# Kernel tuning notes

Hardware: AMD Instinct MI355X
Metric: run time of the kernel (lower is better)

Reference implementation:

```python
import jax, jax.numpy as jnp
import numpy as np

B, TD, ND, FD, H = 16384, 256, 256, 512, 8
HID = [512, 256]


def _ln(x, g, b, eps=1e-5):
    m = jnp.mean(x, -1, keepdims=True)
    v = jnp.mean((x - m) ** 2, -1, keepdims=True)
    return (x - m) * jax.lax.rsqrt(v + eps) * g + b


def _mha1(q_in, k_in, v_in, wq, bq, wk, bk, wv, bv, wo, bo):
    # MultiheadAttention with seq_len=1 on both sides; eval mode (dropout off).
    Bq, E = q_in.shape
    dh = E // H
    q = (q_in @ wq.T + bq).reshape(Bq, H, dh)
    k = (k_in @ wk.T + bk).reshape(Bq, H, dh)
    scores = jnp.sum(q * k, -1) / np.sqrt(dh)          # [B, H]
    w = jax.nn.softmax(scores[..., None], axis=-1)      # [B, H, 1] -> exactly 1 (single key)
    attn = jnp.mean(w, axis=1)[:, None, :]              # averaged over heads -> [B, 1, 1]
    v = v_in @ wv.T + bv                                # attn weight == 1, so attn_out == v
    out = v @ wo.T + bo
    return out, attn


def setup_inputs():
    key = jax.random.key(0)
    ks = iter(jax.random.split(key, 40))
    def p(*shape):
        return jax.random.normal(next(ks), shape, dtype=jnp.float32) * 0.02
    inp = {
        'text_emb': jax.random.normal(next(ks), (B, TD), dtype=jnp.float32),
        'num_emb': jax.random.normal(next(ks), (B, ND), dtype=jnp.float32),
        'tp_w': p(FD, TD), 'tp_b': p(FD),
        'np_w': p(FD, ND), 'np_b': p(FD),
        'a1_wq': p(FD, FD), 'a1_wk': p(FD, FD), 'a1_wv': p(FD, FD),
        'a1_bq': p(FD), 'a1_bk': p(FD), 'a1_bv': p(FD),
        'a1_wo': p(FD, FD), 'a1_bo': p(FD),
        'a2_wq': p(FD, FD), 'a2_wk': p(FD, FD), 'a2_wv': p(FD, FD),
        'a2_bq': p(FD), 'a2_bk': p(FD), 'a2_bv': p(FD),
        'a2_wo': p(FD, FD), 'a2_bo': p(FD),
        'n1_g': jnp.ones((FD,), jnp.float32), 'n1_b': jnp.zeros((FD,), jnp.float32),
        'n2_g': jnp.ones((FD,), jnp.float32), 'n2_b': jnp.zeros((FD,), jnp.float32),
        'g_w': p(FD, 2 * FD), 'g_b': p(FD),
        'm1_w': p(HID[0], 2 * FD), 'm1_b': p(HID[0]),
        'ln1_g': jnp.ones((HID[0],), jnp.float32), 'ln1_b': jnp.zeros((HID[0],), jnp.float32),
        'm2_w': p(HID[1], HID[0]), 'm2_b': p(HID[1]),
        'ln2_g': jnp.ones((HID[1],), jnp.float32), 'ln2_b': jnp.zeros((HID[1],), jnp.float32),
    }
    return inp


def reference(text_emb, num_emb, tp_w, tp_b, np_w, np_b,
              a1_wq, a1_wk, a1_wv, a1_bq, a1_bk, a1_bv, a1_wo, a1_bo,
              a2_wq, a2_wk, a2_wv, a2_bq, a2_bk, a2_bv, a2_wo, a2_bo,
              n1_g, n1_b, n2_g, n2_b, g_w, g_b,
              m1_w, m1_b, ln1_g, ln1_b, m2_w, m2_b, ln2_g, ln2_b):
    t = text_emb @ tp_w.T + tp_b                        # [B, FD]
    n = num_emb @ np_w.T + np_b                         # [B, FD]
    n2t, attn_n2t = _mha1(n, t, t, a1_wq, a1_bq, a1_wk, a1_bk, a1_wv, a1_bv, a1_wo, a1_bo)
    n2t = _ln(n + n2t, n1_g, n1_b)
    t2n, attn_t2n = _mha1(t, n, n, a2_wq, a2_bq, a2_wk, a2_bk, a2_wv, a2_bv, a2_wo, a2_bo)
    t2n = _ln(t + t2n, n2_g, n2_b)
    comb = jnp.concatenate([n2t, t2n], axis=-1)         # [B, 2*FD]
    gate = jax.nn.sigmoid(comb @ g_w.T + g_b)           # [B, FD]
    h = jax.nn.gelu(_ln(comb @ m1_w.T + m1_b, ln1_g, ln1_b), approximate=False)
    fused = jax.nn.gelu(_ln(h @ m2_w.T + m2_b, ln2_g, ln2_b), approximate=False)
    return fused, gate, attn_n2t, attn_t2n
```

## Files before the change

kernel.cpp:

```cpp
#include <hip/hip_runtime.h>
#include <math.h>

typedef unsigned short u16;
typedef __bf16 bf16x8 __attribute__((ext_vector_type(8)));
typedef float f32x4 __attribute__((ext_vector_type(4)));
typedef short s16x8 __attribute__((ext_vector_type(8)));
typedef short s16x4 __attribute__((ext_vector_type(4)));

__device__ __forceinline__ float b2f(u16 u) {
    union { unsigned i; float f; } c; c.i = ((unsigned)u) << 16; return c.f;
}
__device__ __forceinline__ u16 f2b(float f) {
    union { float f; unsigned i; } c; c.f = f;
    return (u16)((c.i + 0x7fffu + ((c.i >> 16) & 1u)) >> 16);
}
__device__ __forceinline__ float gelu_f(float v) {
    return 0.5f * v * (1.0f + erff(v * 0.70710678118654752f));
}
__device__ __forceinline__ void async_cp16(const u16* g, u16* l) {
    __builtin_amdgcn_global_load_lds((const __attribute__((address_space(1))) void*)g,
                                     (__attribute__((address_space(3))) void*)l, 16, 0, 0);
}

__global__ __launch_bounds__(512, 2)
void gemm_big(const u16* __restrict__ A0, const u16* __restrict__ A1,
              const u16* __restrict__ W0, const u16* __restrict__ W1,
              const float* __restrict__ B0, const float* __restrict__ B1,
              const float* __restrict__ LG0, const float* __restrict__ LB0,
              const float* __restrict__ LG1, const float* __restrict__ LB1,
              void* __restrict__ O0v, void* __restrict__ O1v,
              int lda, int K, int ldo0, int ldo1, int mode0, int mode1)
{
    __shared__ u16 sm[(128 + 512) * 64];
    u16* sA = sm;
    u16* sW = sm + 128 * 64;

    const int half = blockIdx.x;
    const int by = blockIdx.y;
    const u16* A = (half ? A1 : A0) + (size_t)by * 128 * lda;
    const u16* W = half ? W1 : W0;
    const float* bias = half ? B1 : B0;
    const float* lng = half ? LG1 : LG0;
    const float* lnb = half ? LB1 : LB0;
    void* outv = half ? O1v : O0v;
    const int ldo = half ? ldo1 : ldo0;
    const int mode = half ? mode1 : mode0;

    const int tid = threadIdx.x;
    const int lane = tid & 63;
    const int wave = tid >> 6;
    const int wrow = wave >> 2;
    const int wcol = wave & 3;
    const int fc = lane & 15;
    const int quad = lane >> 4;

    int par[2], pac[2];
#pragma unroll
    for (int c = 0; c < 2; ++c) {
        const int p = tid + 512 * c;
        par[c] = p >> 3;
        pac[c] = ((p & 7) - (par[c] & 7)) & 7;
    }
    int pwr[8], pwc[8];
#pragma unroll
    for (int c = 0; c < 8; ++c) {
        const int p = tid + 512 * c;
        pwr[c] = p >> 3;
        pwc[c] = ((p & 7) - (pwr[c] & 7)) & 7;
    }

    f32x4 acc[4][8];
#pragma unroll
    for (int i = 0; i < 4; ++i)
#pragma unroll
        for (int j = 0; j < 8; ++j)
            acc[i][j] = f32x4{0.f, 0.f, 0.f, 0.f};

    for (int k0 = 0; k0 < K; k0 += 64) {
#pragma unroll
        for (int c = 0; c < 2; ++c)
            async_cp16(A + (size_t)par[c] * lda + k0 + pac[c] * 8, &sA[(tid + 512 * c) * 8]);
#pragma unroll
        for (int c = 0; c < 8; ++c)
            async_cp16(W + (size_t)pwr[c] * K + k0 + pwc[c] * 8, &sW[(tid + 512 * c) * 8]);
        __syncthreads();

#pragma unroll
        for (int kk = 0; kk < 2; ++kk) {
            bf16x8 af[4];
#pragma unroll
            for (int i = 0; i < 4; ++i) {
                const int ar = wrow * 64 + i * 16 + fc;
                const int slot = ar * 8 + ((kk * 4 + quad + (ar & 7)) & 7);
                af[i] = *(const bf16x8*)&sA[slot * 8];
            }
            bf16x8 wf[8];
#pragma unroll
            for (int j = 0; j < 8; ++j) {
                const int wr = wcol * 128 + j * 16 + fc;
                const int slot = wr * 8 + ((kk * 4 + quad + (wr & 7)) & 7);
                wf[j] = *(const bf16x8*)&sW[slot * 8];
            }
#pragma unroll
            for (int i = 0; i < 4; ++i)
#pragma unroll
            for (int j = 0; j < 8; ++j)
                acc[i][j] =
                    __builtin_amdgcn_mfma_f32_16x16x32_bf16(af[i], wf[j], acc[i][j], 0, 0, 0);
        }
        __syncthreads();
    }

    float bb[8];
#pragma unroll
    for (int j = 0; j < 8; ++j)
        bb[j] = bias[wcol * 128 + j * 16 + fc];

    if (mode == 1) {
        float* smf = (float*)sm;
#pragma unroll
        for (int p = 0; p < 4; ++p) {
            if (wrow == (p >> 1)) {
#pragma unroll
                for (int i2 = 0; i2 < 2; ++i2) {
                    const int i = 2 * (p & 1) + i2;
#pragma unroll
                    for (int j = 0; j < 8; ++j) {
                        const int col = wcol * 128 + j * 16 + fc;
#pragma unroll
                        for (int r = 0; r < 4; ++r) {
                            const int lr = i2 * 16 + quad * 4 + r;
                            smf[lr * 516 + col] =
                                1.0f / (1.0f + expf(-(acc[i][j][r] + bb[j])));
                        }
                    }
                }
            }
            __syncthreads();
            const int rl = tid >> 4, c0 = (tid & 15) * 32;
            const int grow = by * 128 + p * 32 + rl;
            float* o = (float*)outv;
#pragma unroll
            for (int k = 0; k < 8; ++k)
                *(f32x4*)&o[(size_t)grow * ldo + c0 + 4 * k] =
                    *(const f32x4*)&smf[rl * 516 + c0 + 4 * k];
            __syncthreads();
        }
    } else {
        float gv[8], bvv[8];
#pragma unroll
        for (int e = 0; e < 8; ++e) {
            gv[e] = lng[lane * 8 + e];
            bvv[e] = lnb[lane * 8 + e];
        }
#pragma unroll
        for (int p = 0; p < 2; ++p) {
            if (wrow == p) {
#pragma unroll
                for (int i = 0; i < 4; ++i)
#pragma unroll
                for (int j = 0; j < 8; ++j) {
                    const int col = wcol * 128 + j * 16 + fc;
#pragma unroll
                    for (int r = 0; r < 4; ++r) {
                        const int lr = i * 16 + quad * 4 + r;
                        sm[lr * 520 + col] = f2b(acc[i][j][r] + bb[j]);
                    }
                }
            }
            __syncthreads();
            for (int rr = 0; rr < 8; ++rr) {
                const int rl = wave * 8 + rr;
                const int grow = by * 128 + p * 64 + rl;
                float x[8], s = 0.f, ss = 0.f;
                s16x8 xv = *(const s16x8*)&sm[rl * 520 + lane * 8];
#pragma unroll
                for (int e = 0; e < 8; ++e) { x[e] = b2f((u16)xv[e]); s += x[e]; ss += x[e] * x[e]; }
#pragma unroll
                for (int m = 32; m >= 1; m >>= 1) { s += __shfl_xor(s, m, 64); ss += __shfl_xor(ss, m, 64); }
                const float mean = s * (1.f / 512.f);
                const float var = ss * (1.f / 512.f) - mean * mean;
                const float rs = rsqrtf(var + 1e-5f);
                s16x8 ov;
#pragma unroll
                for (int e = 0; e < 8; ++e) {
                    float y = (x[e] - mean) * rs * gv[e] + bvv[e];
                    if (mode == 3) y = gelu_f(y);
                    ov[e] = (short)f2b(y);
                }
                *(s16x8*)&((u16*)outv)[(size_t)grow * ldo + lane * 8] = ov;
            }
            __syncthreads();
        }
    }
}

template<int SUBN, int IR>
__global__ __launch_bounds__(256, 2)
void gemm_bt(const u16* __restrict__ A0, const u16* __restrict__ A1,
             const u16* __restrict__ W0, const u16* __restrict__ W1,
             const float* __restrict__ B0, const float* __restrict__ B1,
             const float* __restrict__ LG0, const float* __restrict__ LB0,
             const float* __restrict__ LG1, const float* __restrict__ LB1,
             void* __restrict__ O0v, void* __restrict__ O1v,
             int lda, int K, int halfBlocks, int ldo0, int ldo1,
             int mode0, int mode1)
{
    constexpr int BM   = IR * 16;
    constexpr int NCOL = 256 * SUBN;
    constexpr int WCH  = 8 * SUBN;
    constexpr int EPIW = NCOL + 8;
    constexpr int STAGEU = (BM + NCOL) * 64;
    constexpr int EPIS = (IR == 4) ? 64 * EPIW : 0;
    __shared__ u16 sm[(STAGEU > EPIS) ? STAGEU : EPIS];
    u16* sA = sm;
    u16* sW = sm + BM * 64;

    const int bx = blockIdx.x, by = blockIdx.y;
    const int half = (bx >= halfBlocks) ? 1 : 0;
    const int bxl = bx - half * halfBlocks;
    const u16* A = (half ? A1 : A0) + (size_t)by * BM * lda;
    const u16* W = (half ? W1 : W0) + (size_t)bxl * NCOL * K;
    const float* bias = half ? B1 : B0;
    const float* lng = half ? LG1 : LG0;
    const float* lnb = half ? LB1 : LB0;
    void* outv = half ? O1v : O0v;
    const int ldo = half ? ldo1 : ldo0;
    const int mode = half ? mode1 : mode0;

    const int tid = threadIdx.x;
    const int lane = tid & 63;
    const int wave = tid >> 6;
    const int fc = lane & 15;
    const int quad = lane >> 4;

    int par[2], pac[2];
#pragma unroll
    for (int c = 0; c < 2; ++c) {
        const int p = tid + 256 * c;
        par[c] = p >> 3;
        pac[c] = ((p & 7) - (par[c] & 7)) & 7;
    }
    int pwr[WCH], pwc[WCH];
#pragma unroll
    for (int c = 0; c < WCH; ++c) {
        const int p = tid + 256 * c;
        pwr[c] = p >> 3;
        pwc[c] = ((p & 7) - (pwr[c] & 7)) & 7;
    }

    f32x4 acc[IR][4 * SUBN];
#pragma unroll
    for (int i = 0; i < IR; ++i)
#pragma unroll
        for (int j = 0; j < 4 * SUBN; ++j)
            acc[i][j] = f32x4{0.f, 0.f, 0.f, 0.f};

    for (int k0 = 0; k0 < K; k0 += 64) {
#pragma unroll
        for (int c = 0; c < 2; ++c) {
            const int p = tid + 256 * c;
            if (p < BM * 8)
                async_cp16(A + (size_t)par[c] * lda + k0 + pac[c] * 8, &sA[p * 8]);
        }
#pragma unroll
        for (int c = 0; c < WCH; ++c)
            async_cp16(W + (size_t)pwr[c] * K + k0 + pwc[c] * 8,
                       &sW[(tid + 256 * c) * 8]);
        __syncthreads();

#pragma unroll
        for (int kk = 0; kk < 2; ++kk) {
            bf16x8 af[IR];
#pragma unroll
            for (int i = 0; i < IR; ++i) {
                const int ar = i * 16 + fc;
                const int slot = ar * 8 + ((kk * 4 + quad + (ar & 7)) & 7);
                af[i] = *(const bf16x8*)&sA[slot * 8];
            }
#pragma unroll
            for (int sub = 0; sub < SUBN; ++sub) {
                bf16x8 wf[4];
#pragma unroll
                for (int j = 0; j < 4; ++j) {
                    const int wr = wave * 64 * SUBN + sub * 64 + j * 16 + fc;
                    const int slot = wr * 8 + ((kk * 4 + quad + (wr & 7)) & 7);
                    wf[j] = *(const bf16x8*)&sW[slot * 8];
                }
#pragma unroll
                for (int i = 0; i < IR; ++i)
#pragma unroll
                    for (int j = 0; j < 4; ++j)
                        acc[i][sub * 4 + j] =
                            __builtin_amdgcn_mfma_f32_16x16x32_bf16(af[i], wf[j], acc[i][sub * 4 + j], 0, 0, 0);
            }
        }
        __syncthreads();
    }

    const int colb = bxl * NCOL;

    if (mode <= 1) {
#pragma unroll
        for (int sub = 0; sub < SUBN; ++sub)
#pragma unroll
        for (int j = 0; j < 4; ++j) {
            const int colh = colb + wave * 64 * SUBN + sub * 64 + j * 16 + fc;
            const float bv = bias[colh];
#pragma unroll
            for (int i = 0; i < IR; ++i)
#pragma unroll
            for (int r = 0; r < 4; ++r) {
                const int row = by * BM + i * 16 + quad * 4 + r;
                const float v = acc[i][sub * 4 + j][r] + bv;
                if (mode == 1)
                    ((float*)outv)[(size_t)row * ldo + colh] = 1.0f / (1.0f + expf(-v));
                else
                    ((u16*)outv)[(size_t)row * ldo + colh] = f2b(v);
            }
        }
    } else if constexpr (IR == 4) {
        float bb[SUBN * 4];
#pragma unroll
        for (int sub = 0; sub < SUBN; ++sub)
#pragma unroll
        for (int j = 0; j < 4; ++j)
            bb[sub * 4 + j] = bias[colb + wave * 64 * SUBN + sub * 64 + j * 16 + fc];
#pragma unroll
        for (int sub = 0; sub < SUBN; ++sub)
#pragma unroll
        for (int j = 0; j < 4; ++j) {
            const int col = wave * 64 * SUBN + sub * 64 + j * 16 + fc;
#pragma unroll
            for (int i = 0; i < 4; ++i)
#pragma unroll
            for (int r = 0; r < 4; ++r)
                sm[(i * 16 + quad * 4 + r) * EPIW + col] =
                    f2b(acc[i][sub * 4 + j][r] + bb[sub * 4 + j]);
        }
        __syncthreads();

        constexpr int CE = NCOL / 64;
        constexpr float INV = 1.0f / (float)NCOL;
        float gv[CE], bvv[CE];
#pragma unroll
        for (int e = 0; e < CE; ++e) {
            gv[e] = lng[lane * CE + e];
            bvv[e] = lnb[lane * CE + e];
        }
        for (int rr = 0; rr < 16; ++rr) {
            const int rl = wave * 16 + rr;
            const int grow = by * 64 + rl;
            float x[CE], s = 0.f, ss = 0.f;
            if constexpr (CE == 8) {
                s16x8 xv = *(const s16x8*)&sm[rl * EPIW + lane * 8];
#pragma unroll
                for (int e = 0; e < 8; ++e) { x[e] = b2f((u16)xv[e]); s += x[e]; ss += x[e] * x[e]; }
            } else {
                s16x4 xv = *(const s16x4*)&sm[rl * EPIW + lane * 4];
#pragma unroll
                for (int e = 0; e < 4; ++e) { x[e] = b2f((u16)xv[e]); s += x[e]; ss += x[e] * x[e]; }
            }
#pragma unroll
            for (int m = 32; m >= 1; m >>= 1) { s += __shfl_xor(s, m, 64); ss += __shfl_xor(ss, m, 64); }
            const float mean = s * INV;
            const float var = ss * INV - mean * mean;
            const float rs = rsqrtf(var + 1e-5f);
            float y[CE];
#pragma unroll
            for (int e = 0; e < CE; ++e) {
                y[e] = (x[e] - mean) * rs * gv[e] + bvv[e];
                if (mode >= 3) y[e] = gelu_f(y[e]);
            }
            if (mode == 4) {
                float* o = (float*)outv;
#pragma unroll
                for (int e = 0; e < CE; ++e)
                    o[(size_t)grow * ldo + colb + lane * CE + e] = y[e];
                if (lane == 0) {
                    o[(size_t)16384 * 768 + grow] = 1.0f;
                    o[(size_t)16384 * 769 + grow] = 1.0f;
                }
            } else {
                u16* o = (u16*)outv;
                if constexpr (CE == 8) {
                    s16x8 ov;
#pragma unroll
                    for (int e = 0; e < 8; ++e) ov[e] = (short)f2b(y[e]);
                    *(s16x8*)&o[(size_t)grow * ldo + colb + lane * 8] = ov;
                } else {
                    s16x4 ov;
#pragma unroll
                    for (int e = 0; e < 4; ++e) ov[e] = (short)f2b(y[e]);
                    *(s16x4*)&o[(size_t)grow * ldo + colb + lane * 4] = ov;
                }
            }
        }
    }
}


__device__ __forceinline__ void cvt_quads(const float* __restrict__ src,
                                          u16* __restrict__ dst, int bi, int tid)
{
#pragma unroll
    for (int c = 0; c < 2; ++c) {
        const int q = bi * 512 + tid + 256 * c;
        f32x4 v = *(const f32x4*)(src + (size_t)q * 4);
        s16x4 o;
        o[0] = (short)f2b(v[0]); o[1] = (short)f2b(v[1]);
        o[2] = (short)f2b(v[2]); o[3] = (short)f2b(v[3]);
        *(s16x4*)(dst + (size_t)q * 4) = o;
    }
}

__device__ void transpose_cvt64(const float* __restrict__ src, int C,
                                u16* __restrict__ dst, int R,
                                int tr, int tc, int tid, float* sm)
{
    const int lr = tid >> 4, lc4 = (tid & 15) * 4;
#pragma unroll
    for (int m = 0; m < 4; ++m) {
        const int i = lr + m * 16;
        f32x4 v = *(const f32x4*)&src[(size_t)(tr + i) * C + tc + lc4];
#pragma unroll
        for (int mm = 0; mm < 4; ++mm) sm[i * 65 + lc4 + mm] = v[mm];
    }
    __syncthreads();
#pragma unroll
    for (int m = 0; m < 4; ++m) {
        const int j = lr + m * 16;
        s16x4 o;
#pragma unroll
        for (int mm = 0; mm < 4; ++mm)
            o[mm] = (short)f2b(sm[(size_t)(lc4 + mm) * 65 + j]);
        *(s16x4*)&dst[(size_t)(tc + j) * R + tr + lc4] = o;
    }
}

__device__ void matvec_rows(const float* __restrict__ M, const float* __restrict__ v,
                            const float* __restrict__ add1, const float* __restrict__ add2,
                            float* __restrict__ out, int r0, int tid, float* sm)
{
    for (int i = tid; i < 512; i += 256) sm[i] = v[i];
    __syncthreads();
    const int row = r0 + (tid & 63), q = tid >> 6;
    float s = 0.f;
    for (int k = q * 128; k < q * 128 + 128; k += 4) {
        f32x4 m = *(const f32x4*)&M[(size_t)row * 512 + k];
        s += m[0] * sm[k] + m[1] * sm[k + 1] + m[2] * sm[k + 2] + m[3] * sm[k + 3];
    }
    sm[512 + tid] = s;
    __syncthreads();
    if (tid < 64)
        out[r0 + tid] = sm[512 + tid] + sm[512 + tid + 64] + sm[512 + tid + 128] +
                        sm[512 + tid + 192] + add1[r0 + tid] + add2[r0 + tid];
}

__global__ __launch_bounds__(256)
void prep_cvt(const float* __restrict__ text, const float* __restrict__ num,
              const float* __restrict__ tp_w, const float* __restrict__ np_w,
              const float* __restrict__ g_w, const float* __restrict__ m1_w,
              const float* __restrict__ m2_w,
              const float* __restrict__ a1_wv, const float* __restrict__ a2_wv,
              const float* __restrict__ a1_wo, const float* __restrict__ a2_wo,
              const float* __restrict__ a1_bv, const float* __restrict__ a1_bo,
              const float* __restrict__ a2_bv, const float* __restrict__ a2_bo,
              const float* __restrict__ tp_b, const float* __restrict__ np_b,
              u16* __restrict__ EMBc, u16* __restrict__ Wbig,
              u16* __restrict__ g_bf, u16* __restrict__ m1_bf, u16* __restrict__ m2_bf,
              u16* __restrict__ a1_wvT, u16* __restrict__ a2_wvT,
              u16* __restrict__ tp_wT, u16* __restrict__ np_wT,
              u16* __restrict__ a1_wo_bf, u16* __restrict__ a2_wo_bf,
              float* __restrict__ w1, float* __restrict__ w2,
              float* __restrict__ zb)
{
    __shared__ float smem[64 * 65];
    const int b = blockIdx.x, tid = threadIdx.x;
    if (b < 4096) {
#pragma unroll
        for (int c = 0; c < 2; ++c) {
            const int q = b * 512 + tid + 256 * c;
            const int e = q * 4, row = e >> 9, col = e & 511;
            const float* src = (col < 256) ? text + (size_t)row * 256 + col
                                           : num + (size_t)row * 256 + (col - 256);
            f32x4 v = *(const f32x4*)src;
            s16x4 o;
            o[0] = (short)f2b(v[0]); o[1] = (short)f2b(v[1]);
            o[2] = (short)f2b(v[2]); o[3] = (short)f2b(v[3]);
            *(s16x4*)(EMBc + e) = o;
        }
    } else if (b < 4352) { cvt_quads(g_w, g_bf, b - 4096, tid); }
    else if (b < 4608) { cvt_quads(m1_w, m1_bf, b - 4352, tid); }
    else if (b < 4672) { cvt_quads(m2_w, m2_bf, b - 4608, tid); }
    else if (b < 4736) {
#pragma unroll
        for (int c = 0; c < 2; ++c) {
            const int q = (b - 4672) * 512 + tid + 256 * c;
            const int e = q * 4, row = e >> 8, col = e & 255;
            f32x4 v = *(const f32x4*)(np_w + e);
            s16x4 o;
            o[0] = (short)f2b(v[0]); o[1] = (short)f2b(v[1]);
            o[2] = (short)f2b(v[2]); o[3] = (short)f2b(v[3]);
            *(s16x4*)(Wbig + (size_t)row * 512 + 256 + col) = o;
        }
    } else if (b < 4800) {
#pragma unroll
        for (int c = 0; c < 2; ++c) {
            const int q = (b - 4736) * 512 + tid + 256 * c;
            const int e = q * 4, row = e >> 8, col = e & 255;
            f32x4 v = *(const f32x4*)(tp_w + e);
            s16x4 o;
            o[0] = (short)f2b(v[0]); o[1] = (short)f2b(v[1]);
            o[2] = (short)f2b(v[2]); o[3] = (short)f2b(v[3]);
            *(s16x4*)(Wbig + (size_t)(512 + row) * 512 + col) = o;
        }
    } else if (b < 4864) {
        const int t = b - 4800;
        transpose_cvt64(a1_wv, 512, a1_wvT, 512, (t >> 3) * 64, (t & 7) * 64, tid, smem);
    } else if (b < 4928) {
        const int t = b - 4864;
        transpose_cvt64(a2_wv, 512, a2_wvT, 512, (t >> 3) * 64, (t & 7) * 64, tid, smem);
    } else if (b < 4960) {
        const int t = b - 4928;
        transpose_cvt64(tp_w, 256, tp_wT, 512, (t >> 2) * 64, (t & 3) * 64, tid, smem);
    } else if (b < 4992) {
        const int t = b - 4960;
        transpose_cvt64(np_w, 256, np_wT, 512, (t >> 2) * 64, (t & 3) * 64, tid, smem);
    } else if (b < 5120) { cvt_quads(a1_wo, a1_wo_bf, b - 4992, tid); }
    else if (b < 5248) { cvt_quads(a2_wo, a2_wo_bf, b - 5120, tid); }
    else if (b < 5256) {
        matvec_rows(a1_wo, a1_bv, a1_bo, np_b, w1, (b - 5248) * 64, tid, smem);
    } else if (b < 5264) {
        matvec_rows(a2_wo, a2_bv, a2_bo, tp_b, w2, (b - 5256) * 64, tid, smem);
    } else {
        *(f32x4*)&zb[tid * 4] = f32x4{0.f, 0.f, 0.f, 0.f};
    }
}

__global__ __launch_bounds__(256)
void prep_bias(const u16* __restrict__ M1, const u16* __restrict__ M2,
               const float* __restrict__ tp_b, const float* __restrict__ np_b,
               const float* __restrict__ w1, const float* __restrict__ w2,
               float* __restrict__ bbig)
{
    __shared__ float sm[768];
    const int b = blockIdx.x, tid = threadIdx.x;
    const int side = b >> 3, r0 = (b & 7) * 64;
    const u16* M = side ? M2 : M1;
    const float* v = side ? np_b : tp_b;
    const float* w = side ? w2 : w1;
    float* out = bbig + side * 512;
    for (int i = tid; i < 512; i += 256) sm[i] = v[i];
    __syncthreads();
    const int row = r0 + (tid & 63), q = tid >> 6;
    float s = 0.f;
    for (int k = q * 128; k < q * 128 + 128; k += 8) {
        s16x8 m = *(const s16x8*)&M[(size_t)row * 512 + k];
#pragma unroll
        for (int j = 0; j < 8; ++j) s += b2f((u16)m[j]) * sm[k + j];
    }
    sm[512 + tid] = s;
    __syncthreads();
    if (tid < 64)
        out[r0 + tid] = sm[512 + tid] + sm[512 + tid + 64] + sm[512 + tid + 128] +
                        sm[512 + tid + 192] + w[r0 + tid];
}

extern "C" void kernel_launch(void* const* d_in, const int* in_sizes, int n_in,
                              void* d_out, int out_size, void* d_ws, size_t ws_size,
                              hipStream_t stream)
{
    const float* text  = (const float*)d_in[0];
    const float* num   = (const float*)d_in[1];
    const float* tp_w  = (const float*)d_in[2];
    const float* tp_b  = (const float*)d_in[3];
    const float* np_w  = (const float*)d_in[4];
    const float* np_b  = (const float*)d_in[5];
    const float* a1_wv = (const float*)d_in[8];
    const float* a1_bv = (const float*)d_in[11];
    const float* a1_wo = (const float*)d_in[12];
    const float* a1_bo = (const float*)d_in[13];
    const float* a2_wv = (const float*)d_in[16];
    const float* a2_bv = (const float*)d_in[19];
    const float* a2_wo = (const float*)d_in[20];
    const float* a2_bo = (const float*)d_in[21];
    const float* n1_g  = (const float*)d_in[22];
    const float* n1_b  = (const float*)d_in[23];
    const float* n2_g  = (const float*)d_in[24];
    const float* n2_b  = (const float*)d_in[25];
    const float* g_w   = (const float*)d_in[26];
    const float* g_b   = (const float*)d_in[27];
    const float* m1_w  = (const float*)d_in[28];
    const float* m1_b  = (const float*)d_in[29];
    const float* ln1_g = (const float*)d_in[30];
    const float* ln1_b = (const float*)d_in[31];
    const float* m2_w  = (const float*)d_in[32];
    const float* m2_b  = (const float*)d_in[33];
    const float* ln2_g = (const float*)d_in[34];
    const float* ln2_b = (const float*)d_in[35];

    float* outp = (float*)d_out;
    char* ob = (char*)d_out;
    char* ws = (char*)d_ws;
    const size_t KB = 1024, MB = 1048576;

    u16* Wbig    = (u16*)(ob);
    u16* g_bf    = (u16*)(ob + 1 * MB);
    u16* m1_bf   = (u16*)(ob + 2 * MB);
    u16* a1_wvT  = (u16*)(ob + 3 * MB + 256 * KB);
    u16* a2_wvT  = (u16*)(ob + 3 * MB + 768 * KB);
    u16* tp_wT   = (u16*)(ob + 4 * MB + 256 * KB);
    u16* np_wT   = (u16*)(ob + 4 * MB + 512 * KB);
    u16* a1_wo_bf= (u16*)(ob + 4 * MB + 768 * KB);
    u16* a2_wo_bf= (u16*)(ob + 5 * MB + 256 * KB);
    u16* M1      = (u16*)(ob + 5 * MB + 768 * KB);
    u16* M2      = (u16*)(ob + 6 * MB + 256 * KB);
    float* w1    = (float*)(ob + 6 * MB + 768 * KB);
    float* w2    = w1 + 512;
    float* bbig  = w1 + 1024;
    float* zb    = w1 + 2048;
    u16* EMBc    = (u16*)(ob + 16 * MB);
    u16* X     = (u16*)ws;
    u16* m2_bf = (u16*)(ws + 32 * MB);
    u16* h     = (u16*)(ws + 48 * MB);

    dim3 blk(256);

    prep_cvt<<<5265, blk, 0, stream>>>(text, num, tp_w, np_w, g_w, m1_w, m2_w,
        a1_wv, a2_wv, a1_wo, a2_wo, a1_bv, a1_bo, a2_bv, a2_bo, tp_b, np_b,
        EMBc, Wbig, g_bf, m1_bf, m2_bf, a1_wvT, a2_wvT, tp_wT, np_wT,
        a1_wo_bf, a2_wo_bf, w1, w2, zb);
    gemm_bt<1, 1><<<dim3(4, 32), blk, 0, stream>>>(a1_wo_bf, a2_wo_bf, a1_wvT, a2_wvT,
        zb, zb, nullptr, nullptr, nullptr, nullptr,
        M1, M2, 512, 512, 2, 512, 512, 0, 0);
    prep_bias<<<16, blk, 0, stream>>>(M1, M2, tp_b, np_b, w1, w2, bbig);
    gemm_bt<1, 1><<<dim3(2, 32), blk, 0, stream>>>(M1, M2, tp_wT, np_wT,
        zb, zb, nullptr, nullptr, nullptr, nullptr,
        Wbig, Wbig + (size_t)512 * 512 + 256, 512, 512, 1, 512, 512, 0, 0);
    gemm_big<<<dim3(2, 128), dim3(512), 0, stream>>>(EMBc, EMBc,
        Wbig, Wbig + (size_t)512 * 512, bbig, bbig + 512,
        n1_g, n1_b, n2_g, n2_b,
        X, X + 512, 512, 512, 1024, 1024, 2, 2);
    gemm_big<<<dim3(2, 128), dim3(512), 0, stream>>>(X, X, g_bf, m1_bf, g_b, m1_b,
        nullptr, nullptr, ln1_g, ln1_b,
        outp + (size_t)16384 * 256, h, 1024, 1024, 512, 512, 1, 3);
    gemm_bt<1, 4><<<dim3(1, 256), blk, 0, stream>>>(h, h, m2_bf, m2_bf, m2_b, m2_b,
        ln2_g, ln2_b, ln2_g, ln2_b,
        outp, outp, 512, 512, 1, 256, 256, 4, 4);
}
```

Measured before the change: 315.9 us.

## Double-buffer gemm_big LDS with K=32 tiles and phased prefetch interleaved with MFMA

Rewrites the main big GEMM to use two LDS buffers holding 32-wide K tiles. Async global-to-LDS copies for the next tile are spread across four MFMA phases, with barriers and setprio guarding each phase, so the loads overlap the math instead of waiting on a sync before compute. The epilogues are reworked to use smaller staging chunks that fit the new LDS footprint. The risks are extra barrier overhead per phase and an LDS swizzle that is new and must stay correct.

```diff
diff --git a/kernel.cpp b/kernel.cpp
--- a/kernel.cpp
+++ b/kernel.cpp
@@ -23,7 +23,7 @@
 }
 
 __global__ __launch_bounds__(512, 2)
-void gemm_big(const u16* __restrict__ A0, const u16* __restrict__ A1,
+void gemm_8ph(const u16* __restrict__ A0, const u16* __restrict__ A1,
               const u16* __restrict__ W0, const u16* __restrict__ W1,
               const float* __restrict__ B0, const float* __restrict__ B1,
               const float* __restrict__ LG0, const float* __restrict__ LB0,
@@ -31,9 +31,7 @@
               void* __restrict__ O0v, void* __restrict__ O1v,
               int lda, int K, int ldo0, int ldo1, int mode0, int mode1)
 {
-    __shared__ u16 sm[(128 + 512) * 64];
-    u16* sA = sm;
-    u16* sW = sm + 128 * 64;
+    __shared__ u16 smem[2 * 20480];
 
     const int half = blockIdx.x;
     const int by = blockIdx.y;
@@ -54,19 +52,28 @@
     const int fc = lane & 15;
     const int quad = lane >> 4;
 
-    int par[2], pac[2];
-#pragma unroll
-    for (int c = 0; c < 2; ++c) {
+    int sar, sac;
+    { const int hi = tid >> 3, t7 = ((tid & 7) - hi) & 7; sar = 2 * hi + (t7 >> 2); sac = t7 & 3; }
+    int swr[4], swc[4];
+#pragma unroll
+    for (int c = 0; c < 4; ++c) {
         const int p = tid + 512 * c;
-        par[c] = p >> 3;
-        pac[c] = ((p & 7) - (par[c] & 7)) & 7;
-    }
-    int pwr[8], pwc[8];
-#pragma unroll
-    for (int c = 0; c < 8; ++c) {
-        const int p = tid + 512 * c;
-        pwr[c] = p >> 3;
-        pwc[c] = ((p & 7) - (pwr[c] & 7)) & 7;
+        const int hi = p >> 3, t7 = ((p & 7) - hi) & 7;
+        swr[c] = 2 * hi + (t7 >> 2); swc[c] = t7 & 3;
+    }
+    int aoff[4];
+#pragma unroll
+    for (int i = 0; i < 4; ++i) {
+        const int r = wrow * 64 + i * 16 + fc;
+        const int s = ((r >> 1) << 3) + ((((r & 1) << 2) + quad + (r >> 1)) & 7);
+        aoff[i] = s * 8;
+    }
+    int woff[8];
+#pragma unroll
+    for (int jj = 0; jj < 8; ++jj) {
+        const int r = wcol * 128 + jj * 16 + fc;
+        const int s = ((r >> 1) << 3) + ((((r & 1) << 2) + quad + (r >> 1)) & 7);
+        woff[jj] = s * 8;
     }
 
     f32x4 acc[4][8];
@@ -76,104 +83,122 @@
         for (int j = 0; j < 8; ++j)
             acc[i][j] = f32x4{0.f, 0.f, 0.f, 0.f};
 
-    for (int k0 = 0; k0 < K; k0 += 64) {
-#pragma unroll
-        for (int c = 0; c < 2; ++c)
-            async_cp16(A + (size_t)par[c] * lda + k0 + pac[c] * 8, &sA[(tid + 512 * c) * 8]);
-#pragma unroll
-        for (int c = 0; c < 8; ++c)
-            async_cp16(W + (size_t)pwr[c] * K + k0 + pwc[c] * 8, &sW[(tid + 512 * c) * 8]);
-        __syncthreads();
-
-#pragma unroll
-        for (int kk = 0; kk < 2; ++kk) {
-            bf16x8 af[4];
+    const int NT = K >> 5;
+    async_cp16(A + (size_t)sar * lda + sac * 8, smem + tid * 8);
+#pragma unroll
+    for (int c = 0; c < 4; ++c)
+        async_cp16(W + (size_t)swr[c] * K + swc[c] * 8, smem + 4096 + (tid + 512 * c) * 8);
+    asm volatile("s_waitcnt vmcnt(0)" ::: "memory");
+    __builtin_amdgcn_s_barrier();
+    __builtin_amdgcn_sched_barrier(0);
+
+    for (int t = 0; t < NT; ++t) {
+        const int cur = t & 1;
+        const u16* bA = smem + cur * 20480;
+        const u16* bW = bA + 4096;
+        u16* nbase = smem + (cur ^ 1) * 20480;
+        const int nk = (t + 1) << 5;
+        const bool pf = (t + 1 < NT);
+
+        bf16x8 af[4];
+#pragma unroll
+        for (int i = 0; i < 4; ++i) af[i] = *(const bf16x8*)&bA[aoff[i]];
+
+#pragma unroll
+        for (int p = 0; p < 4; ++p) {
+            bf16x8 wfa = *(const bf16x8*)&bW[woff[2 * p]];
+            bf16x8 wfb = *(const bf16x8*)&bW[woff[2 * p + 1]];
+            if (pf) {
+                if (p == 0) {
+                    async_cp16(A + (size_t)sar * lda + nk + sac * 8, nbase + tid * 8);
+                    async_cp16(W + (size_t)swr[0] * K + nk + swc[0] * 8,
+                               nbase + 4096 + tid * 8);
+                    async_cp16(W + (size_t)swr[1] * K + nk + swc[1] * 8,
+                               nbase + 4096 + (tid + 512) * 8);
+                } else if (p == 1) {
+                    async_cp16(W + (size_t)swr[2] * K + nk + swc[2] * 8,
+                               nbase + 4096 + (tid + 1024) * 8);
+                } else if (p == 2) {
+                    async_cp16(W + (size_t)swr[3] * K + nk + swc[3] * 8,
+                               nbase + 4096 + (tid + 1536) * 8);
+                }
+            }
+            __builtin_amdgcn_s_barrier();
+            asm volatile("s_waitcnt lgkmcnt(0)" ::: "memory");
+            __builtin_amdgcn_sched_barrier(0);
+            __builtin_amdgcn_s_setprio(1);
 #pragma unroll
             for (int i = 0; i < 4; ++i) {
-                const int ar = wrow * 64 + i * 16 + fc;
-                const int slot = ar * 8 + ((kk * 4 + quad + (ar & 7)) & 7);
-                af[i] = *(const bf16x8*)&sA[slot * 8];
-            }
-            bf16x8 wf[8];
-#pragma unroll
-            for (int j = 0; j < 8; ++j) {
-                const int wr = wcol * 128 + j * 16 + fc;
-                const int slot = wr * 8 + ((kk * 4 + quad + (wr & 7)) & 7);
-                wf[j] = *(const bf16x8*)&sW[slot * 8];
-            }
-#pragma unroll
-            for (int i = 0; i < 4; ++i)
-#pragma unroll
-            for (int j = 0; j < 8; ++j)
-                acc[i][j] =
-                    __builtin_amdgcn_mfma_f32_16x16x32_bf16(af[i], wf[j], acc[i][j], 0, 0, 0);
-        }
-        __syncthreads();
+                acc[i][2 * p] =
+                    __builtin_amdgcn_mfma_f32_16x16x32_bf16(af[i], wfa, acc[i][2 * p], 0, 0, 0);
+                acc[i][2 * p + 1] =
+                    __builtin_amdgcn_mfma_f32_16x16x32_bf16(af[i], wfb, acc[i][2 * p + 1], 0, 0, 0);
+            }
+            __builtin_amdgcn_s_setprio(0);
+            if (p == 3 && pf)
+                asm volatile("s_waitcnt vmcnt(0)" ::: "memory");
+            __builtin_amdgcn_s_barrier();
+            __builtin_amdgcn_sched_barrier(0);
+        }
     }
 
     float bb[8];
 #pragma unroll
-    for (int j = 0; j < 8; ++j)
-        bb[j] = bias[wcol * 128 + j * 16 + fc];
+    for (int jj = 0; jj < 8; ++jj)
+        bb[jj] = bias[wcol * 128 + jj * 16 + fc];
 
     if (mode == 1) {
-        float* smf = (float*)sm;
-#pragma unroll
-        for (int p = 0; p < 4; ++p) {
-            if (wrow == (p >> 1)) {
-#pragma unroll
-                for (int i2 = 0; i2 < 2; ++i2) {
-                    const int i = 2 * (p & 1) + i2;
-#pragma unroll
-                    for (int j = 0; j < 8; ++j) {
-                        const int col = wcol * 128 + j * 16 + fc;
-#pragma unroll
-                        for (int r = 0; r < 4; ++r) {
-                            const int lr = i2 * 16 + quad * 4 + r;
-                            smf[lr * 516 + col] =
-                                1.0f / (1.0f + expf(-(acc[i][j][r] + bb[j])));
-                        }
-                    }
+        float* sf = (float*)smem;
+        for (int q = 0; q < 8; ++q) {
+            if (wrow == (q >> 2)) {
+                const int i = q & 3;
+#pragma unroll
+                for (int jj = 0; jj < 8; ++jj) {
+                    const int col = wcol * 128 + jj * 16 + fc;
+#pragma unroll
+                    for (int r = 0; r < 4; ++r)
+                        sf[(quad * 4 + r) * 516 + col] =
+                            1.0f / (1.0f + expf(-(acc[i][jj][r] + bb[jj])));
                 }
             }
             __syncthreads();
-            const int rl = tid >> 4, c0 = (tid & 15) * 32;
-            const int grow = by * 128 + p * 32 + rl;
             float* o = (float*)outv;
 #pragma unroll
-            for (int k = 0; k < 8; ++k)
-                *(f32x4*)&o[(size_t)grow * ldo + c0 + 4 * k] =
-                    *(const f32x4*)&smf[rl * 516 + c0 + 4 * k];
+            for (int it = 0; it < 4; ++it) {
+                const int rl = it * 4 + (tid >> 7);
+                const int cidx = (tid & 127) * 4;
+                const int grow = by * 128 + q * 16 + rl;
+                *(f32x4*)&o[(size_t)grow * ldo + cidx] = *(const f32x4*)&sf[rl * 516 + cidx];
+            }
             __syncthreads();
         }
     } else {
-        float gv[8], bvv[8];
+        float gv[8], bv8[8];
 #pragma unroll
         for (int e = 0; e < 8; ++e) {
             gv[e] = lng[lane * 8 + e];
-            bvv[e] = lnb[lane * 8 + e];
-        }
-#pragma unroll
-        for (int p = 0; p < 2; ++p) {
-            if (wrow == p) {
-#pragma unroll
-                for (int i = 0; i < 4; ++i)
-#pragma unroll
-                for (int j = 0; j < 8; ++j) {
-                    const int col = wcol * 128 + j * 16 + fc;
-#pragma unroll
-                    for (int r = 0; r < 4; ++r) {
-                        const int lr = i * 16 + quad * 4 + r;
-                        sm[lr * 520 + col] = f2b(acc[i][j][r] + bb[j]);
-                    }
+            bv8[e] = lnb[lane * 8 + e];
+        }
+        for (int q = 0; q < 4; ++q) {
+            if (wrow == (q >> 1)) {
+                const int i0 = 2 * (q & 1);
+#pragma unroll
+                for (int i2 = 0; i2 < 2; ++i2)
+#pragma unroll
+                for (int jj = 0; jj < 8; ++jj) {
+                    const int col = wcol * 128 + jj * 16 + fc;
+#pragma unroll
+                    for (int r = 0; r < 4; ++r)
+                        smem[(i2 * 16 + quad * 4 + r) * 520 + col] =
+                            f2b(acc[i0 + i2][jj][r] + bb[jj]);
                 }
             }
             __syncthreads();
-            for (int rr = 0; rr < 8; ++rr) {
-                const int rl = wave * 8 + rr;
-                const int grow = by * 128 + p * 64 + rl;
+            for (int rr = 0; rr < 4; ++rr) {
+                const int rl = wave * 4 + rr;
+                const int grow = by * 128 + q * 32 + rl;
                 float x[8], s = 0.f, ss = 0.f;
-                s16x8 xv = *(const s16x8*)&sm[rl * 520 + lane * 8];
+                s16x8 xv = *(const s16x8*)&smem[rl * 520 + lane * 8];
 #pragma unroll
                 for (int e = 0; e < 8; ++e) { x[e] = b2f((u16)xv[e]); s += x[e]; ss += x[e] * x[e]; }
 #pragma unroll
@@ -184,7 +209,7 @@
                 s16x8 ov;
 #pragma unroll
                 for (int e = 0; e < 8; ++e) {
-                    float y = (x[e] - mean) * rs * gv[e] + bvv[e];
+                    float y = (x[e] - mean) * rs * gv[e] + bv8[e];
                     if (mode == 3) y = gelu_f(y);
                     ov[e] = (short)f2b(y);
                 }
@@ -638,11 +663,11 @@
     gemm_bt<1, 1><<<dim3(2, 32), blk, 0, stream>>>(M1, M2, tp_wT, np_wT,
         zb, zb, nullptr, nullptr, nullptr, nullptr,
         Wbig, Wbig + (size_t)512 * 512 + 256, 512, 512, 1, 512, 512, 0, 0);
-    gemm_big<<<dim3(2, 128), dim3(512), 0, stream>>>(EMBc, EMBc,
+    gemm_8ph<<<dim3(2, 128), dim3(512), 0, stream>>>(EMBc, EMBc,
         Wbig, Wbig + (size_t)512 * 512, bbig, bbig + 512,
         n1_g, n1_b, n2_g, n2_b,
         X, X + 512, 512, 512, 1024, 1024, 2, 2);
-    gemm_big<<<dim3(2, 128), dim3(512), 0, stream>>>(X, X, g_bf, m1_bf, g_b, m1_b,
+    gemm_8ph<<<dim3(2, 128), dim3(512), 0, stream>>>(X, X, g_bf, m1_bf, g_b, m1_b,
         nullptr, nullptr, ln1_g, ln1_b,
         outp + (size_t)16384 * 256, h, 1024, 1024, 512, 512, 1, 3);
     gemm_bt<1, 4><<<dim3(1, 256), blk, 0, stream>>>(h, h, m2_bf, m2_bf, m2_b, m2_b,
```

Measured after the change: 355.0 us. +12.4%, slower.
